# Kernel optimization log

Hardware: AMD Instinct MI355X
Metric: run time of the kernel (lower is better)

Reference implementation:

```python
import jax, jax.numpy as jnp
import numpy as np

N = 4096
INP_DIM = 256
EMB_DIM = 256
ALPHA = 0.01  # LeakyReLU negative slope
NEG_INF = -9.0e15


def _xavier(key, shape, gain=1.414):
    fan_in, fan_out = shape[0], shape[1]
    limit = gain * np.sqrt(6.0 / (fan_in + fan_out))
    return jax.random.uniform(key, shape, jnp.float32, -limit, limit)


def setup_inputs() -> dict:
    key = jax.random.key(0)
    ks = jax.random.split(key, 9)
    inp = {
        "input": jax.random.normal(ks[0], (N, INP_DIM), jnp.float32),
        "adj": jax.random.randint(ks[1], (N, N), 0, 2, jnp.int32),
        "W0": _xavier(ks[2], (INP_DIM, EMB_DIM)),
        "W1": _xavier(ks[3], (EMB_DIM, EMB_DIM)),
        "a1": _xavier(ks[4], (2 * EMB_DIM, 1)),
        "W2": _xavier(ks[5], (EMB_DIM, EMB_DIM)),
        "a2": _xavier(ks[6], (2 * EMB_DIM, 1)),
        "W3": _xavier(ks[7], (EMB_DIM, EMB_DIM)),
        "a3": _xavier(ks[8], (2 * EMB_DIM, 1)),
    }
    return inp


def _gat_layer(h, adj, W, a):
    # h: [N, F_in], W: [F_in, F], a: [2F, 1]
    Wh = h @ W                       # [N, F]
    F_out = Wh.shape[1]
    # e_ij = leakyrelu([Wh_i || Wh_j] @ a) = leakyrelu(Wh_i@a1 + Wh_j@a2)
    f1 = Wh @ a[:F_out]              # [N, 1]
    f2 = Wh @ a[F_out:]              # [N, 1]
    e = jax.nn.leaky_relu(f1 + f2.T, ALPHA)            # [N, N]
    att = jnp.where(adj > 0, e, NEG_INF)
    att = jax.nn.softmax(att, axis=1)                    # masked softmax over neighbors
    h_prime = att @ Wh                                   # [N, F]
    return jax.nn.elu(h_prime)                           # concat=True -> ELU


def reference(input, adj, W0, W1, a1, W2, a2, W3, a3):
    h = input @ W0                   # GAT-level projection
    h = _gat_layer(h, adj, W1, a1)
    h = _gat_layer(h, adj, W2, a2)
    h = _gat_layer(h, adj, W3, a3)
    return h
```

## Files before the change

kernel.cpp:

```cpp
#include <hip/hip_runtime.h>
#include <hip/hip_bf16.h>
#include <cstdint>
#include <cstddef>

#define NN 4096
#define FD 256
#define WPR 64

typedef __attribute__((ext_vector_type(8))) unsigned short ushort8v;
typedef __attribute__((ext_vector_type(4))) unsigned short ushort4v;
typedef __attribute__((ext_vector_type(8))) short short8;
typedef __attribute__((ext_vector_type(4))) float float4v;

#define C1 30.0f
#define C2 0.3f

static __device__ __forceinline__ unsigned short f2bf(float x) {
    union { float f; unsigned int u; } v; v.f = x;
    unsigned int r = v.u + 0x7FFFu + ((v.u >> 16) & 1u);
    return (unsigned short)(r >> 16);
}

static __device__ __forceinline__ short8 as_s8(ushort8v v) {
    union { ushort8v u; short8 s; } x; x.u = v; return x.s;
}

__global__ __launch_bounds__(256) void setup(const int* __restrict__ adj,
                                             const float* __restrict__ input,
                                             const float* __restrict__ W0, const float* __restrict__ W1,
                                             const float* __restrict__ W2, const float* __restrict__ W3,
                                             unsigned long long* __restrict__ bits,
                                             unsigned short* __restrict__ hb,
                                             unsigned short* __restrict__ Wbt,
                                             float* __restrict__ f1f2) {
    const int b = blockIdx.x;
    const int t = threadIdx.x;
    if (b < 4096) {
        const int wave = t >> 6, lane = t & 63;
        const int* arow = adj + (size_t)b * NN;
        #pragma unroll
        for (int it = 0; it < NN / 256; ++it) {
            int j = it * 256 + wave * 64 + lane;
            unsigned long long m = __ballot(arow[j] > 0);
            if (lane == 0) bits[(size_t)b * WPR + (it * 4 + wave)] = m;
        }
        hb[(size_t)b * 256 + t] = f2bf(input[(size_t)b * 256 + t]);
    } else if (b < 5120) {
        int idx = (b - 4096) * 256 + t;
        int mat = idx >> 16;
        int within = idx & 65535;
        int n = within >> 8, k = within & 255;
        const float* W = (mat == 0) ? W0 : (mat == 1) ? W1 : (mat == 2) ? W2 : W3;
        Wbt[idx] = f2bf(W[k * 256 + n]);
    } else {
        #pragma unroll
        for (int i = 0; i < 24; ++i) {
            int pos = i * 1024 + (b - 5120) * 256 + t;
            f1f2[pos] = 0.f;
        }
    }
}

__global__ __launch_bounds__(256) void proj_gemm(const unsigned short* __restrict__ A,
                                                 const unsigned short* __restrict__ Bt,
                                                 const float* __restrict__ av,
                                                 float* __restrict__ f1f2,
                                                 unsigned short* __restrict__ Cbt,
                                                 unsigned short* __restrict__ Crow) {
    const int t = threadIdx.x;
    const int bm = blockIdx.x >> 2, bn = blockIdx.x & 3;
    const int m0 = bm * 64, n0 = bn * 64;
    __shared__ unsigned short As[64 * 264];
    __shared__ unsigned short Bs[64 * 264];
    const int lane = t & 63, wave = t >> 6;
    const int wm = (wave >> 1) * 32, wn = (wave & 1) * 32;
    const int lr = t >> 2, lc0 = (t & 3) * 8;
    #pragma unroll
    for (int i = 0; i < 8; ++i) {
        int col = lc0 + i * 32;
        *(ushort8v*)&As[lr * 264 + col] = *(const ushort8v*)&A[(size_t)(m0 + lr) * 256 + col];
        *(ushort8v*)&Bs[lr * 264 + col] = *(const ushort8v*)&Bt[(size_t)(n0 + lr) * 256 + col];
    }
    __syncthreads();
    float4v acc[2][2] = {{{0.f,0.f,0.f,0.f},{0.f,0.f,0.f,0.f}},{{0.f,0.f,0.f,0.f},{0.f,0.f,0.f,0.f}}};
    #pragma unroll
    for (int kk = 0; kk < 256; kk += 32) {
        const int kc = kk + (lane >> 4) * 8;
        #pragma unroll
        for (int fm = 0; fm < 2; ++fm) {
            short8 a = as_s8(*(const ushort8v*)&As[(wm + fm * 16 + (lane & 15)) * 264 + kc]);
            #pragma unroll
            for (int fn = 0; fn < 2; ++fn) {
                short8 b = as_s8(*(const ushort8v*)&Bs[(wn + fn * 16 + (lane & 15)) * 264 + kc]);
                acc[fm][fn] = __builtin_amdgcn_mfma_f32_16x16x32_bf16(a, b, acc[fm][fn], 0, 0, 0);
            }
        }
    }

    const int rb = wm + (lane >> 4) * 4;
    const int cb = wn + (lane & 15);
    if (Crow) {
        #pragma unroll
        for (int fm = 0; fm < 2; ++fm)
            #pragma unroll
            for (int fn = 0; fn < 2; ++fn)
                #pragma unroll
                for (int r = 0; r < 4; ++r)
                    Crow[(size_t)(m0 + rb + fm * 16 + r) * 256 + n0 + cb + fn * 16] = f2bf(acc[fm][fn][r]);
    }

    if (f1f2) {
        float a1c[2], a2c[2];
        #pragma unroll
        for (int fn = 0; fn < 2; ++fn) {
            a1c[fn] = av[n0 + cb + fn * 16];
            a2c[fn] = av[256 + n0 + cb + fn * 16];
        }
        #pragma unroll
        for (int fm = 0; fm < 2; ++fm)
            #pragma unroll
            for (int r = 0; r < 4; ++r) {
                float s1 = acc[fm][0][r] * a1c[0] + acc[fm][1][r] * a1c[1];
                float s2 = acc[fm][0][r] * a2c[0] + acc[fm][1][r] * a2c[1];
                #pragma unroll
                for (int off = 1; off < 16; off <<= 1) {
                    s1 += __shfl_xor(s1, off, 64);
                    s2 += __shfl_xor(s2, off, 64);
                }
                if ((lane & 15) == 0) {
                    int row = m0 + rb + fm * 16 + r;
                    atomicAdd(&f1f2[row], s1);
                    atomicAdd(&f1f2[4096 + row], s2);
                }
            }
    }

    if (Cbt) {
        unsigned short* T = As;
        __syncthreads();
        #pragma unroll
        for (int fm = 0; fm < 2; ++fm)
            #pragma unroll
            for (int fn = 0; fn < 2; ++fn)
                #pragma unroll
                for (int r = 0; r < 4; ++r)
                    T[(cb + fn * 16) * 72 + rb + fm * 16 + r] = f2bf(acc[fm][fn][r]);
        __syncthreads();
        const int tr = t >> 2;
        #pragma unroll
        for (int i = 0; i < 2; ++i) {
            int tc = (t & 3) * 8 + i * 32;
            *(ushort8v*)&Cbt[(size_t)(n0 + tr) * 4096 + m0 + tc] = *(const ushort8v*)&T[tr * 72 + tc];
        }
    }
}

__global__ __launch_bounds__(256) void rowcoef(const unsigned long long* __restrict__ bits,
                                               const float* __restrict__ f1f2,
                                               float4* __restrict__ rowco) {
    __shared__ float2 tl[4096];
    const int t = threadIdx.x;
    const float* f2p = f1f2 + 4096;
    #pragma unroll
    for (int i = 0; i < 16; ++i) {
        float v = f2p[i * 256 + t];
        tl[i * 256 + t] = make_float2(__expf(v - C1), __expf(0.01f * v - C2));
    }
    __syncthreads();
    const int lane = t & 63, wave = t >> 6;
    for (int rr = 0; rr < 2; ++rr) {
        const int row = blockIdx.x * 8 + wave * 2 + rr;
        const unsigned long long wl = bits[(size_t)row * WPR + lane];
        const float f1r = f1f2[row];
        const float th = __expf(-f1r - C1);
        float mx = 0.f, S1 = 0.f, S2 = 0.f;
        #pragma unroll 16
        for (int b = 0; b < 64; ++b) {
            unsigned long long w = __shfl(wl, b, 64);
            bool bit = (w >> lane) & 1ULL;
            float2 v = tl[b * 64 + lane];
            float ebm = bit ? v.x : 0.f;
            mx = fmaxf(mx, ebm);
            bool cond = v.x > th;
            S1 += (bit && cond)  ? v.x : 0.f;
            S2 += (bit && !cond) ? v.y : 0.f;
        }
        #pragma unroll
        for (int off = 1; off < 64; off <<= 1) {
            mx = fmaxf(mx, __shfl_xor(mx, off, 64));
            S1 += __shfl_xor(S1, off, 64);
            S2 += __shfl_xor(S2, off, 64);
        }
        if (lane == 0) {
            float M  = C1 + __logf(mx);
            float fm_ = f1r + M;
            float m  = fm_ > 0.f ? fm_ : 0.01f * fm_;
            float alpha = __expf(fminf(f1r + C1 - m, 60.f));
            float gamma = __expf(fminf(0.01f * (f1r + C1) - m, 60.f));
            float inv = 1.0f / (alpha * S1 + gamma * S2);
            rowco[row] = make_float4(alpha * inv, gamma * inv, -f1r, 0.f);
        }
    }
}

__global__ __launch_bounds__(256, 2) void att_split(const unsigned long long* __restrict__ bits,
                                                    const float4* __restrict__ rowco,
                                                    const float* __restrict__ f1f2,
                                                    const unsigned short* __restrict__ Bt,
                                                    float* __restrict__ part, int kchunk) {
    const int t = threadIdx.x;
    const int bm = blockIdx.x & 63;
    const int ks = blockIdx.x >> 6;
    const int m0 = bm * 64;
    const int k0 = ks * kchunk;
    __shared__ unsigned short As[64 * 72];
    const int lane = t & 63, wave = t >> 6;
    const int wn = wave * 64;
    const int sr = t >> 2, sc = (t & 3) * 16;
    const float4 rc = rowco[m0 + sr];
    const float pA = rc.x, pG = rc.y, thf2 = rc.z;
    const unsigned long long* brow = bits + (size_t)(m0 + sr) * WPR;
    const float* f2p = f1f2 + 4096;
    const unsigned short* bbase = Bt + (size_t)(wn + (lane & 15)) * 4096 + (lane >> 4) * 8;
    float4v acc[4][4];
    #pragma unroll
    for (int i = 0; i < 4; ++i)
        #pragma unroll
        for (int j = 0; j < 4; ++j) acc[i][j] = (float4v){0.f, 0.f, 0.f, 0.f};

    for (int kk = k0; kk < k0 + kchunk; kk += 64) {
        const unsigned int wb = (unsigned int)(brow[kk >> 6] >> sc) & 0xFFFFu;
        float fv[16];
        {
            const float4v* fp = (const float4v*)&f2p[kk + sc];
            #pragma unroll
            for (int i = 0; i < 4; ++i) {
                float4v x = fp[i];
                fv[4 * i] = x[0]; fv[4 * i + 1] = x[1]; fv[4 * i + 2] = x[2]; fv[4 * i + 3] = x[3];
            }
        }
        ushort8v pa0, pa1;
        #pragma unroll
        for (int jj = 0; jj < 16; ++jj) {
            float f2j = fv[jj];
            bool cond = f2j > thf2;
            float arg  = cond ? (f2j - C1) : (0.01f * f2j - C2);
            float coef = cond ? pA : pG;
            float p = ((wb >> jj) & 1u) ? coef * __expf(arg) : 0.f;
            unsigned short pb = f2bf(p);
            if (jj < 8) pa0[jj] = pb; else pa1[jj - 8] = pb;
        }
        *(ushort8v*)&As[sr * 72 + sc]     = pa0;
        *(ushort8v*)&As[sr * 72 + sc + 8] = pa1;
        ushort8v breg[4][2];
        #pragma unroll
        for (int fn = 0; fn < 4; ++fn)
            #pragma unroll
            for (int half = 0; half < 2; ++half)
                breg[fn][half] = *(const ushort8v*)&bbase[(size_t)(fn * 16) * 4096 + kk + half * 32];
        __syncthreads();
        #pragma unroll
        for (int half = 0; half < 2; ++half) {
            const int kc = half * 32 + (lane >> 4) * 8;
            short8 a[4];
            #pragma unroll
            for (int fm = 0; fm < 4; ++fm)
                a[fm] = as_s8(*(const ushort8v*)&As[(fm * 16 + (lane & 15)) * 72 + kc]);
            #pragma unroll
            for (int fm = 0; fm < 4; ++fm)
                #pragma unroll
                for (int fn = 0; fn < 4; ++fn)
                    acc[fm][fn] = __builtin_amdgcn_mfma_f32_16x16x32_bf16(a[fm], as_s8(breg[fn][half]), acc[fm][fn], 0, 0, 0);
        }
        __syncthreads();
    }

    const int rb = (lane >> 4) * 4;
    const int cb = wn + (lane & 15);
    float* pbase = part + ((size_t)ks << 20);
    #pragma unroll
    for (int fm = 0; fm < 4; ++fm)
        #pragma unroll
        for (int fn = 0; fn < 4; ++fn)
            #pragma unroll
            for (int r = 0; r < 4; ++r)
                pbase[(size_t)(m0 + rb + fm * 16 + r) * 256 + cb + fn * 16] = acc[fm][fn][r];
}

__global__ __launch_bounds__(256) void att_reduce(const float* __restrict__ part,
                                                  float* __restrict__ outf,
                                                  unsigned short* __restrict__ hrow, int nsplit) {
    const int idx = (blockIdx.x * 256 + threadIdx.x) * 4;
    float4v s = *(const float4v*)&part[idx];
    for (int sp = 1; sp < nsplit; ++sp)
        s += *(const float4v*)&part[((size_t)sp << 20) + idx];
    float4v v;
    ushort4v hb;
    #pragma unroll
    for (int j = 0; j < 4; ++j) {
        float x = s[j];
        x = x > 0.f ? x : (__expf(x) - 1.f);
        v[j] = x;
        hb[j] = f2bf(x);
    }
    if (outf) *(float4v*)&outf[idx] = v;
    *(ushort4v*)&hrow[idx] = hb;
}

extern "C" void kernel_launch(void* const* d_in, const int* in_sizes, int n_in,
                              void* d_out, int out_size, void* d_ws, size_t ws_size,
                              hipStream_t stream) {
    const float* input = (const float*)d_in[0];
    const int*   adj   = (const int*)d_in[1];
    const float* W0    = (const float*)d_in[2];
    const float* W1    = (const float*)d_in[3];
    const float* a1    = (const float*)d_in[4];
    const float* W2    = (const float*)d_in[5];
    const float* a2    = (const float*)d_in[6];
    const float* W3    = (const float*)d_in[7];
    const float* a3    = (const float*)d_in[8];
    float* out = (float*)d_out;
    char* ws = (char*)d_ws;

    unsigned long long* bits = (unsigned long long*)(ws);
    unsigned short* h0   = (unsigned short*)(ws + (2u << 20));
    unsigned short* h1   = (unsigned short*)(ws + (4u << 20));
    unsigned short* Whbt = (unsigned short*)(ws + (6u << 20));
    unsigned short* Wbt  = (unsigned short*)(ws + (8u << 20));
    float*  f1f2  = (float*)(ws + (9u << 20));
    float4* rowco = (float4*)(ws + (10u << 20));
    float*  part  = (float*)(ws + (13u << 20));

    const size_t base = 13u << 20;
    int SPLIT = 8;
    while (SPLIT > 1 && base + (size_t)SPLIT * (4u << 20) > ws_size) SPLIT >>= 1;
    const int kchunk = NN / SPLIT;

    float* f1f2_l[3] = { f1f2, f1f2 + 8192, f1f2 + 16384 };

    setup<<<5124, 256, 0, stream>>>(adj, input, W0, W1, W2, W3, bits, h0, Wbt, f1f2);

    proj_gemm<<<256, 256, 0, stream>>>(h0, Wbt + 0 * 65536, nullptr, nullptr, nullptr, h1);

    proj_gemm<<<256, 256, 0, stream>>>(h1, Wbt + 1 * 65536, a1, f1f2_l[0], Whbt, nullptr);
    rowcoef<<<512, 256, 0, stream>>>(bits, f1f2_l[0], rowco);
    att_split<<<64 * SPLIT, 256, 0, stream>>>(bits, rowco, f1f2_l[0], Whbt, part, kchunk);
    att_reduce<<<1024, 256, 0, stream>>>(part, nullptr, h0, SPLIT);

    proj_gemm<<<256, 256, 0, stream>>>(h0, Wbt + 2 * 65536, a2, f1f2_l[1], Whbt, nullptr);
    rowcoef<<<512, 256, 0, stream>>>(bits, f1f2_l[1], rowco);
    att_split<<<64 * SPLIT, 256, 0, stream>>>(bits, rowco, f1f2_l[1], Whbt, part, kchunk);
    att_reduce<<<1024, 256, 0, stream>>>(part, nullptr, h1, SPLIT);

    proj_gemm<<<256, 256, 0, stream>>>(h1, Wbt + 3 * 65536, a3, f1f2_l[2], Whbt, nullptr);
    rowcoef<<<512, 256, 0, stream>>>(bits, f1f2_l[2], rowco);
    att_split<<<64 * SPLIT, 256, 0, stream>>>(bits, rowco, f1f2_l[2], Whbt, part, kchunk);
    att_reduce<<<1024, 256, 0, stream>>>(part, out, h0, SPLIT);
}
```

Before: 287.2 us.

## Build attention A-fragments in registers from precomputed exp table, drop LDS staging

```diff
diff --git a/kernel.cpp b/kernel.cpp
--- a/kernel.cpp
+++ b/kernel.cpp
@@ -157,14 +157,17 @@
 
 __global__ __launch_bounds__(256) void rowcoef(const unsigned long long* __restrict__ bits,
                                                const float* __restrict__ f1f2,
-                                               float4* __restrict__ rowco) {
+                                               float4* __restrict__ rowco,
+                                               float2* __restrict__ tab2g) {
     __shared__ float2 tl[4096];
     const int t = threadIdx.x;
     const float* f2p = f1f2 + 4096;
     #pragma unroll
     for (int i = 0; i < 16; ++i) {
         float v = f2p[i * 256 + t];
-        tl[i * 256 + t] = make_float2(__expf(v - C1), __expf(0.01f * v - C2));
+        float2 pr = make_float2(__expf(v - C1), __expf(0.01f * v - C2));
+        tl[i * 256 + t] = pr;
+        if (blockIdx.x == 0) tab2g[i * 256 + t] = pr;
     }
     __syncthreads();
     const int lane = t & 63, wave = t >> 6;
@@ -198,30 +201,34 @@
             float alpha = __expf(fminf(f1r + C1 - m, 60.f));
             float gamma = __expf(fminf(0.01f * (f1r + C1) - m, 60.f));
             float inv = 1.0f / (alpha * S1 + gamma * S2);
-            rowco[row] = make_float4(alpha * inv, gamma * inv, -f1r, 0.f);
-        }
-    }
-}
-
-__global__ __launch_bounds__(256, 2) void att_split(const unsigned long long* __restrict__ bits,
-                                                    const float4* __restrict__ rowco,
-                                                    const float* __restrict__ f1f2,
-                                                    const unsigned short* __restrict__ Bt,
-                                                    float* __restrict__ part, int kchunk) {
+            rowco[row] = make_float4(alpha * inv, gamma * inv, th, 0.f);
+        }
+    }
+}
+
+__global__ __launch_bounds__(256, 2) void att_flat(const unsigned long long* __restrict__ bits,
+                                                   const float4* __restrict__ rowco,
+                                                   const float2* __restrict__ tab2,
+                                                   const unsigned short* __restrict__ Bt,
+                                                   float* __restrict__ part, int kchunk) {
     const int t = threadIdx.x;
     const int bm = blockIdx.x & 63;
     const int ks = blockIdx.x >> 6;
     const int m0 = bm * 64;
     const int k0 = ks * kchunk;
-    __shared__ unsigned short As[64 * 72];
     const int lane = t & 63, wave = t >> 6;
     const int wn = wave * 64;
-    const int sr = t >> 2, sc = (t & 3) * 16;
-    const float4 rc = rowco[m0 + sr];
-    const float pA = rc.x, pG = rc.y, thf2 = rc.z;
-    const unsigned long long* brow = bits + (size_t)(m0 + sr) * WPR;
-    const float* f2p = f1f2 + 4096;
-    const unsigned short* bbase = Bt + (size_t)(wn + (lane & 15)) * 4096 + (lane >> 4) * 8;
+    const int g = lane >> 4, ml = lane & 15;
+
+    float pA[4], pG[4], thE[4];
+    #pragma unroll
+    for (int fm = 0; fm < 4; ++fm) {
+        float4 rc = rowco[m0 + fm * 16 + ml];
+        pA[fm] = rc.x; pG[fm] = rc.y; thE[fm] = rc.z;
+    }
+    const unsigned long long* bitb = bits + (size_t)(m0 + ml) * WPR;
+    const unsigned short* bbase = Bt + (size_t)(wn + ml) * 4096 + g * 8;
+
     float4v acc[4][4];
     #pragma unroll
     for (int i = 0; i < 4; ++i)
@@ -229,54 +236,52 @@
         for (int j = 0; j < 4; ++j) acc[i][j] = (float4v){0.f, 0.f, 0.f, 0.f};
 
     for (int kk = k0; kk < k0 + kchunk; kk += 64) {
-        const unsigned int wb = (unsigned int)(brow[kk >> 6] >> sc) & 0xFFFFu;
-        float fv[16];
-        {
-            const float4v* fp = (const float4v*)&f2p[kk + sc];
+        const int word = kk >> 6;
+        unsigned long long w64[4];
+        #pragma unroll
+        for (int fm = 0; fm < 4; ++fm) w64[fm] = bitb[(size_t)(fm * 16) * WPR + word];
+        ushort8v breg[4][2];
+        #pragma unroll
+        for (int fn = 0; fn < 4; ++fn)
+            #pragma unroll
+            for (int h = 0; h < 2; ++h)
+                breg[fn][h] = *(const ushort8v*)&bbase[(size_t)(fn * 16) * 4096 + kk + h * 32];
+
+        #pragma unroll
+        for (int h = 0; h < 2; ++h) {
+            float tb[8], td[8];
+            const float4v* q = (const float4v*)&tab2[kk + h * 32 + g * 8];
             #pragma unroll
             for (int i = 0; i < 4; ++i) {
-                float4v x = fp[i];
-                fv[4 * i] = x[0]; fv[4 * i + 1] = x[1]; fv[4 * i + 2] = x[2]; fv[4 * i + 3] = x[3];
+                float4v v = q[i];
+                tb[2 * i] = v[0]; td[2 * i] = v[1]; tb[2 * i + 1] = v[2]; td[2 * i + 1] = v[3];
             }
-        }
-        ushort8v pa0, pa1;
-        #pragma unroll
-        for (int jj = 0; jj < 16; ++jj) {
-            float f2j = fv[jj];
-            bool cond = f2j > thf2;
-            float arg  = cond ? (f2j - C1) : (0.01f * f2j - C2);
-            float coef = cond ? pA : pG;
-            float p = ((wb >> jj) & 1u) ? coef * __expf(arg) : 0.f;
-            unsigned short pb = f2bf(p);
-            if (jj < 8) pa0[jj] = pb; else pa1[jj - 8] = pb;
-        }
-        *(ushort8v*)&As[sr * 72 + sc]     = pa0;
-        *(ushort8v*)&As[sr * 72 + sc + 8] = pa1;
-        ushort8v breg[4][2];
-        #pragma unroll
-        for (int fn = 0; fn < 4; ++fn)
-            #pragma unroll
-            for (int half = 0; half < 2; ++half)
-                breg[fn][half] = *(const ushort8v*)&bbase[(size_t)(fn * 16) * 4096 + kk + half * 32];
-        __syncthreads();
-        #pragma unroll
-        for (int half = 0; half < 2; ++half) {
-            const int kc = half * 32 + (lane >> 4) * 8;
-            short8 a[4];
+            short8 afr[4];
+            #pragma unroll
+            for (int fm = 0; fm < 4; ++fm) {
+                unsigned int wh = (unsigned int)(w64[fm] >> (h * 32 + g * 8));
+                ushort8v af;
+                #pragma unroll
+                for (int jj = 0; jj < 4; ++jj) {
+                    float e0 = tb[2 * jj], e1 = tb[2 * jj + 1];
+                    float p0 = ((wh >> (2 * jj)) & 1u)     ? (e0 > thE[fm] ? pA[fm] * e0 : pG[fm] * td[2 * jj])     : 0.f;
+                    float p1 = ((wh >> (2 * jj + 1)) & 1u) ? (e1 > thE[fm] ? pA[fm] * e1 : pG[fm] * td[2 * jj + 1]) : 0.f;
+                    union { __hip_bfloat162 b2; unsigned short us[2]; } cv;
+                    cv.b2 = __float22bfloat162_rn(make_float2(p0, p1));
+                    af[2 * jj] = cv.us[0]; af[2 * jj + 1] = cv.us[1];
+                }
+                afr[fm] = as_s8(af);
+            }
             #pragma unroll
             for (int fm = 0; fm < 4; ++fm)
-                a[fm] = as_s8(*(const ushort8v*)&As[(fm * 16 + (lane & 15)) * 72 + kc]);
-            #pragma unroll
-            for (int fm = 0; fm < 4; ++fm)
                 #pragma unroll
                 for (int fn = 0; fn < 4; ++fn)
-                    acc[fm][fn] = __builtin_amdgcn_mfma_f32_16x16x32_bf16(a[fm], as_s8(breg[fn][half]), acc[fm][fn], 0, 0, 0);
-        }
-        __syncthreads();
-    }
-
-    const int rb = (lane >> 4) * 4;
-    const int cb = wn + (lane & 15);
+                    acc[fm][fn] = __builtin_amdgcn_mfma_f32_16x16x32_bf16(afr[fm], as_s8(breg[fn][h]), acc[fm][fn], 0, 0, 0);
+        }
+    }
+
+    const int rb = g * 4;
+    const int cb = wn + ml;
     float* pbase = part + ((size_t)ks << 20);
     #pragma unroll
     for (int fm = 0; fm < 4; ++fm)
@@ -329,6 +334,7 @@
     unsigned short* Wbt  = (unsigned short*)(ws + (8u << 20));
     float*  f1f2  = (float*)(ws + (9u << 20));
     float4* rowco = (float4*)(ws + (10u << 20));
+    float2* tab2  = (float2*)(ws + (10u << 20) + (256u << 10));
     float*  part  = (float*)(ws + (13u << 20));
 
     const size_t base = 13u << 20;
@@ -343,17 +349,17 @@
     proj_gemm<<<256, 256, 0, stream>>>(h0, Wbt + 0 * 65536, nullptr, nullptr, nullptr, h1);
 
     proj_gemm<<<256, 256, 0, stream>>>(h1, Wbt + 1 * 65536, a1, f1f2_l[0], Whbt, nullptr);
-    rowcoef<<<512, 256, 0, stream>>>(bits, f1f2_l[0], rowco);
-    att_split<<<64 * SPLIT, 256, 0, stream>>>(bits, rowco, f1f2_l[0], Whbt, part, kchunk);
+    rowcoef<<<512, 256, 0, stream>>>(bits, f1f2_l[0], rowco, tab2);
+    att_flat<<<64 * SPLIT, 256, 0, stream>>>(bits, rowco, tab2, Whbt, part, kchunk);
     att_reduce<<<1024, 256, 0, stream>>>(part, nullptr, h0, SPLIT);
 
     proj_gemm<<<256, 256, 0, stream>>>(h0, Wbt + 2 * 65536, a2, f1f2_l[1], Whbt, nullptr);
-    rowcoef<<<512, 256, 0, stream>>>(bits, f1f2_l[1], rowco);
-    att_split<<<64 * SPLIT, 256, 0, stream>>>(bits, rowco, f1f2_l[1], Whbt, part, kchunk);
+    rowcoef<<<512, 256, 0, stream>>>(bits, f1f2_l[1], rowco, tab2);
+    att_flat<<<64 * SPLIT, 256, 0, stream>>>(bits, rowco, tab2, Whbt, part, kchunk);
     att_reduce<<<1024, 256, 0, stream>>>(part, nullptr, h1, SPLIT);
 
     proj_gemm<<<256, 256, 0, stream>>>(h1, Wbt + 3 * 65536, a3, f1f2_l[2], Whbt, nullptr);
-    rowcoef<<<512, 256, 0, stream>>>(bits, f1f2_l[2], rowco);
-    att_split<<<64 * SPLIT, 256, 0, stream>>>(bits, rowco, f1f2_l[2], Whbt, part, kchunk);
+    rowcoef<<<512, 256, 0, stream>>>(bits, f1f2_l[2], rowco, tab2);
+    att_flat<<<64 * SPLIT, 256, 0, stream>>>(bits, rowco, tab2, Whbt, part, kchunk);
     att_reduce<<<1024, 256, 0, stream>>>(part, out, h0, SPLIT);
 }
```

Result: slower. 329.6 us (+14.8%).
